# Kernel tuning notes

Hardware: AMD Instinct MI355X
Metric: run time of the kernel (lower is better)

## Reference

```python
import jax, jax.numpy as jnp
import numpy as np

N = 50000        # nodes
E = 1_600_000    # edges (avg degree 32)
H = 4            # attention heads
DPH = 32         # dims per head
D = H * DPH      # hidden/output dim = 128
IN_DIM = 5
NEG_SLOPE = 0.2
LN_EPS = 1e-5


def _glorot(key, shape):
    fan_in = shape[0] if len(shape) > 1 else shape[-1]
    return jax.random.normal(key, shape, jnp.float32) / jnp.sqrt(jnp.float32(fan_in))


def setup_inputs() -> dict:
    key = jax.random.key(0)
    ks = jax.random.split(key, 24)
    inp = {
        'x': jax.random.normal(ks[0], (N, IN_DIM), jnp.float32),
        'w_in': _glorot(ks[1], (IN_DIM, D)),
        'b_in': jnp.zeros((D,), jnp.float32),
    }
    for i in range(3):
        k = 2 + 6 * i
        inp[f'w{i}'] = _glorot(ks[k], (D, D))            # GAT linear
        inp[f'asrc{i}'] = _glorot(ks[k + 1], (H, DPH))   # att_src
        inp[f'adst{i}'] = _glorot(ks[k + 2], (H, DPH))   # att_dst
        inp[f'cb{i}'] = jnp.zeros((D,), jnp.float32)     # conv bias
        inp[f'g{i}'] = jnp.ones((D,), jnp.float32)       # LN gamma
        inp[f'lb{i}'] = jnp.zeros((D,), jnp.float32)     # LN beta
    inp['edge_index'] = jax.random.randint(ks[23], (2, E), 0, N, dtype=jnp.int32)
    return inp


def _gat_layer(h, src, dst, W, a_src, a_dst, bias):
    # h: [N, D]; src/dst: [E+N] (self loops included)
    xh = (h @ W).reshape(N, H, DPH)                      # [N, H, DPH]
    al_s = jnp.einsum('nhd,hd->nh', xh, a_src)           # [N, H]
    al_d = jnp.einsum('nhd,hd->nh', xh, a_dst)
    e = jax.nn.leaky_relu(al_s[src] + al_d[dst], NEG_SLOPE)   # [E', H]
    m = jax.ops.segment_max(e, dst, num_segments=N)      # segment softmax over incoming edges
    ex = jnp.exp(e - m[dst])
    denom = jax.ops.segment_sum(ex, dst, num_segments=N)
    alpha = ex / (denom[dst] + 1e-16)                    # [E', H]
    out = jax.ops.segment_sum(xh[src] * alpha[..., None], dst, num_segments=N)
    return out.reshape(N, D) + bias


def _layer_norm(x, g, b):
    mu = jnp.mean(x, axis=-1, keepdims=True)
    var = jnp.mean((x - mu) ** 2, axis=-1, keepdims=True)
    return (x - mu) * jax.lax.rsqrt(var + LN_EPS) * g + b


def reference(x, w_in, b_in,
              w0, asrc0, adst0, cb0, g0, lb0,
              w1, asrc1, adst1, cb1, g1, lb1,
              w2, asrc2, adst2, cb2, g2, lb2,
              edge_index):
    loops = jnp.arange(N, dtype=edge_index.dtype)
    src = jnp.concatenate([edge_index[0], loops])        # PyG GATConv add_self_loops=True
    dst = jnp.concatenate([edge_index[1], loops])
    h = x @ w_in + b_in                                  # [N, D]
    layers = [(w0, asrc0, adst0, cb0, g0, lb0),
              (w1, asrc1, adst1, cb1, g1, lb1),
              (w2, asrc2, adst2, cb2, g2, lb2)]
    for i, (W, a_s, a_d, cb, g, lb) in enumerate(layers):
        h_new = _gat_layer(h, src, dst, W, a_s, a_d, cb)
        h_new = _layer_norm(h_new, g, lb)
        if i < 2:
            h_new = jax.nn.relu(h_new)                   # dropout = identity in eval
        h = h + h_new                                    # dims always match (128)
    return h
```

## Files before the change

kernel.cpp:

```cpp
#include <hip/hip_runtime.h>

#define NN 50000
#define NE 1600000
#define EP (NE + NN)
#define D 128
#define H 4
#define NEG 0.2f
#define LN_EPS 1e-5f
#define NBUCK 49
#define BCAP 40960
#define CHUNK 4096

typedef _Float16 f16;
typedef _Float16 half8 __attribute__((ext_vector_type(8)));
typedef _Float16 half2v __attribute__((ext_vector_type(2)));
typedef float f32x4v __attribute__((ext_vector_type(4)));
typedef unsigned short u16;
typedef unsigned int u32;

static __device__ __forceinline__ float leakyf(float v) { return fmaxf(v, NEG * v); }

static __device__ __forceinline__ int fkey(float v) {
    int b = __float_as_int(v);
    return b >= 0 ? b : (b ^ 0x7fffffff);
}
static __device__ __forceinline__ float fdec(int k) {
    return __int_as_float(k >= 0 ? k : (k ^ 0x7fffffff));
}
#define NEG_INF_KEY 0x807fffff

__global__ void k_init(int* __restrict__ deg, int* __restrict__ gmaxk,
                       int* __restrict__ gcur,
                       const float* __restrict__ w0, const float* __restrict__ w1,
                       const float* __restrict__ w2, f16* __restrict__ wt,
                       const float* __restrict__ as0, const float* __restrict__ ad0,
                       const float* __restrict__ as1, const float* __restrict__ ad1,
                       const float* __restrict__ as2, const float* __restrict__ ad2,
                       f16* __restrict__ ws16) {
    int t = blockIdx.x * blockDim.x + threadIdx.x;
    if (t < NN) deg[t] = 0;
    if (t < 12) gmaxk[t] = NEG_INF_KEY;
    if (t < NBUCK) gcur[t] = 0;
    int u = t - 50176;
    if (u >= 0 && u < 3 * D * D) {
        int l = u / (D * D), rem = u % (D * D);
        int k = rem >> 7, c = rem & 127;
        const float* w = (l == 0) ? w0 : (l == 1) ? w1 : w2;
        wt[l * D * D + c * D + k] = (f16)w[rem];
    }
    int v = t - 99328;
    if (v >= 0 && v < 3 * 16 * D) {
        int l = v / (16 * D), rem = v % (16 * D);
        int c = rem >> 7, k = rem & 127;
        f16 out = (f16)0.f;
        if (c < 8) {
            int head = c >> 1;
            const float* w = (l == 0) ? w0 : (l == 1) ? w1 : w2;
            const float* av = (c & 1) ? ((l == 0) ? ad0 : (l == 1) ? ad1 : ad2)
                                      : ((l == 0) ? as0 : (l == 1) ? as1 : as2);
            float s = 0.f;
#pragma unroll
            for (int j = 0; j < 32; j++)
                s = fmaf(w[k * D + head * 32 + j], av[head * 32 + j], s);
            out = (f16)s;
        }
        ws16[l * 16 * D + c * D + k] = out;
    }
}

__global__ __launch_bounds__(256) void k_bin(const int* __restrict__ ei,
                                             int* __restrict__ gcur,
                                             u32* __restrict__ binned) {
    __shared__ u32 pk[CHUNK];
    __shared__ int hist[NBUCK], base[NBUCK], lcur[NBUCK];
    int tid = threadIdx.x;
    int cbase = blockIdx.x * CHUNK;
    if (tid < NBUCK) hist[tid] = 0;
    __syncthreads();
#pragma unroll
    for (int j = 0; j < CHUNK / 256; j++) {
        int k = cbase + j * 256 + tid;
        u32 v = 0xFFFFFFFFu;
        if (k < EP) {
            int src, dst;
            if (k < NE) { src = ei[k]; dst = ei[NE + k]; }
            else        { src = k - NE; dst = src; }
            v = ((u32)dst << 16) | (u32)src;
            atomicAdd(&hist[dst >> 10], 1);
        }
        pk[j * 256 + tid] = v;
    }
    __syncthreads();
    if (tid < NBUCK) {
        base[tid] = atomicAdd(&gcur[tid], hist[tid]);
        lcur[tid] = 0;
    }
    __syncthreads();
#pragma unroll
    for (int j = 0; j < CHUNK / 256; j++) {
        u32 v = pk[j * 256 + tid];
        if (v != 0xFFFFFFFFu) {
            int b = v >> 26;
            int pos = base[b] + atomicAdd(&lcur[b], 1);
            binned[(size_t)b * BCAP + pos] = v;
        }
    }
}

__global__ __launch_bounds__(1024) void k_cnt2(const int* __restrict__ gcur,
                                               const u32* __restrict__ binned,
                                               int* __restrict__ deg) {
    __shared__ int hist[1024];
    int b = blockIdx.x >> 2, sub = blockIdx.x & 3;
    hist[threadIdx.x] = 0;
    __syncthreads();
    int cnt = gcur[b];
    const u32* bb = binned + (size_t)b * BCAP;
    for (int i = sub * 1024 + threadIdx.x; i < cnt; i += 4096)
        atomicAdd(&hist[(bb[i] >> 16) & 1023], 1);
    __syncthreads();
    int n = (b << 10) + threadIdx.x;
    if (n < NN && hist[threadIdx.x]) atomicAdd(&deg[n], hist[threadIdx.x]);
}

#define SCAN_B 512
__global__ void k_scan1(const int* __restrict__ deg, int* __restrict__ stmp, int* __restrict__ bsum) {
    __shared__ int sm[SCAN_B];
    int i = blockIdx.x * SCAN_B + threadIdx.x;
    sm[threadIdx.x] = (i < NN) ? ((deg[i] + 7) & ~7) : 0;
    __syncthreads();
    for (int off = 1; off < SCAN_B; off <<= 1) {
        int t = (threadIdx.x >= off) ? sm[threadIdx.x - off] : 0;
        __syncthreads();
        sm[threadIdx.x] += t;
        __syncthreads();
    }
    if (i < NN) stmp[i] = sm[threadIdx.x];
    if (threadIdx.x == SCAN_B - 1) bsum[blockIdx.x] = sm[SCAN_B - 1];
}

__global__ void k_scan2(int* __restrict__ bsum, int nb) {
    __shared__ int sm[256];
    int v = (threadIdx.x < nb) ? bsum[threadIdx.x] : 0;
    sm[threadIdx.x] = v;
    __syncthreads();
    for (int off = 1; off < 256; off <<= 1) {
        int t = (threadIdx.x >= off) ? sm[threadIdx.x - off] : 0;
        __syncthreads();
        sm[threadIdx.x] += t;
        __syncthreads();
    }
    if (threadIdx.x < nb) bsum[threadIdx.x] = sm[threadIdx.x];
}

__global__ void k_scan3(const int* __restrict__ stmp, const int* __restrict__ bsum,
                        const int* __restrict__ deg, int* __restrict__ rowptr,
                        int* __restrict__ cur, u16* __restrict__ csr) {
    int i = blockIdx.x * SCAN_B + threadIdx.x;
    if (i >= NN) return;
    int add = (blockIdx.x > 0) ? bsum[blockIdx.x - 1] : 0;
    int end = stmp[i] + add;
    rowptr[i + 1] = end;
    if (i == 0) rowptr[0] = 0;
    int d = deg[i];
    int start = end - ((d + 7) & ~7);
    cur[i] = start;
    for (int j = start + d; j < end; ++j) csr[j] = 0xFFFFu;
}

__global__ __launch_bounds__(1024) void k_scatter(const int* __restrict__ gcur,
                                                  int* __restrict__ cur,
                                                  const u32* __restrict__ binned,
                                                  u16* __restrict__ csr) {
    int b = blockIdx.x >> 2, sub = blockIdx.x & 3;
    int cnt = gcur[b];
    const u32* bb = binned + (size_t)b * BCAP;
    for (int i = sub * 1024 + threadIdx.x; i < cnt; i += 4096) {
        u32 v = bb[i];
        int dst = v >> 16;
        int pos = atomicAdd(&cur[dst], 1);
        csr[pos] = (u16)(v & 0xFFFFu);
    }
}

__global__ void k_in(const float* __restrict__ x, const float* __restrict__ w,
                     const float* __restrict__ b, f16* __restrict__ h16) {
    int t = blockIdx.x * blockDim.x + threadIdx.x;
    if (t >= NN * D) return;
    int n = t >> 7, d = t & 127;
    const float* xr = x + n * 5;
    float acc = b[d];
#pragma unroll
    for (int k = 0; k < 5; k++) acc = fmaf(xr[k], w[k * D + d], acc);
    h16[t] = (f16)acc;
}

__global__ __launch_bounds__(256) void k_gemm(const f16* __restrict__ h16,
                                              const f16* __restrict__ wt,
                                              const f16* __restrict__ ws16,
                                              f16* __restrict__ xh,
                                              float* __restrict__ als,
                                              float* __restrict__ ald,
                                              int* __restrict__ gmaxk) {
    __shared__ int sgk[4];
    if (threadIdx.x < 4) sgk[threadIdx.x] = NEG_INF_KEY;
    int wid = threadIdx.x >> 6;
    int lane = threadIdx.x & 63;
    int wbase = blockIdx.x * 128 + wid * 32;
    int r = lane & 15;
    int g = lane >> 4;

    int arow0 = wbase + r;      if (arow0 >= NN) arow0 = NN - 1;
    int arow1 = wbase + 16 + r; if (arow1 >= NN) arow1 = NN - 1;
    const f16* a0p = h16 + (size_t)arow0 * D + g * 8;
    const f16* a1p = h16 + (size_t)arow1 * D + g * 8;

    f32x4v acc0[8], acc1[8], al0, al1;
#pragma unroll
    for (int nt = 0; nt < 8; nt++) {
        acc0[nt] = (f32x4v){0.f, 0.f, 0.f, 0.f};
        acc1[nt] = (f32x4v){0.f, 0.f, 0.f, 0.f};
    }
    al0 = (f32x4v){0.f, 0.f, 0.f, 0.f};
    al1 = (f32x4v){0.f, 0.f, 0.f, 0.f};

#pragma unroll
    for (int ks = 0; ks < 4; ks++) {
        half8 a0 = *(const half8*)(a0p + ks * 32);
        half8 a1 = *(const half8*)(a1p + ks * 32);
        half8 bal = *(const half8*)(ws16 + (size_t)r * D + ks * 32 + g * 8);
        al0 = __builtin_amdgcn_mfma_f32_16x16x32_f16(a0, bal, al0, 0, 0, 0);
        al1 = __builtin_amdgcn_mfma_f32_16x16x32_f16(a1, bal, al1, 0, 0, 0);
#pragma unroll
        for (int nt = 0; nt < 8; nt++) {
            half8 b = *(const half8*)(wt + (size_t)(nt * 16 + r) * D + ks * 32 + g * 8);
            acc0[nt] = __builtin_amdgcn_mfma_f32_16x16x32_f16(a0, b, acc0[nt], 0, 0, 0);
            acc1[nt] = __builtin_amdgcn_mfma_f32_16x16x32_f16(a1, b, acc1[nt], 0, 0, 0);
        }
    }

#pragma unroll
    for (int rg = 0; rg < 4; rg++) {
        int n0 = wbase + g * 4 + rg;
        if (n0 < NN) {
#pragma unroll
            for (int nt = 0; nt < 8; nt++)
                xh[(size_t)n0 * D + nt * 16 + r] = (f16)acc0[nt][rg];
        }
        int n1 = wbase + 16 + g * 4 + rg;
        if (n1 < NN) {
#pragma unroll
            for (int nt = 0; nt < 8; nt++)
                xh[(size_t)n1 * D + nt * 16 + r] = (f16)acc1[nt][rg];
        }
    }

    float m = -1e30f;
#pragma unroll
    for (int rg = 0; rg < 4; rg++) {
        int n0 = wbase + g * 4 + rg;
        int n1 = wbase + 16 + g * 4 + rg;
        float v0 = al0[rg], v1 = al1[rg];
        if (r < 8) {
            int hh = r >> 1;
            if (r & 1) {
                if (n0 < NN) ald[n0 * H + hh] = v0;
                if (n1 < NN) ald[n1 * H + hh] = v1;
            } else {
                if (n0 < NN) als[n0 * H + hh] = v0;
                if (n1 < NN) als[n1 * H + hh] = v1;
                m = fmaxf(m, fmaxf(v0, v1));
            }
        }
    }
    m = fmaxf(m, __shfl_xor(m, 16));
    m = fmaxf(m, __shfl_xor(m, 32));
    __syncthreads();
    if (lane < 8 && !(r & 1)) atomicMax(&sgk[r >> 1], fkey(m));
    __syncthreads();
    if (threadIdx.x < 4) atomicMax(&gmaxk[threadIdx.x], sgk[threadIdx.x]);
}

__global__ __launch_bounds__(256) void k_agg(const f16* __restrict__ xh,
                                             const float* __restrict__ als,
                                             const float* __restrict__ ald,
                                             const int* __restrict__ gmaxk,
                                             const int* __restrict__ rp,
                                             const u16* __restrict__ csr,
                                             const float* __restrict__ cb,
                                             const float* __restrict__ gamma,
                                             const float* __restrict__ beta,
                                             f16* __restrict__ h16,
                                             float* __restrict__ hout, int do_relu) {
    int node = blockIdx.x * 4 + (threadIdx.x >> 6);
    if (node >= NN) return;
    int lane = threadIdx.x & 63;
    int slot = lane >> 4;
    int q = lane & 15;
    int head = q >> 2;
    unsigned qo = q * 8;

    int start = rp[node], end = rp[node + 1];

    float adH = ald[node * H + head];
    float mH = leakyf(fdec(gmaxk[head]) + adH);

    float acc[8];
#pragma unroll
    for (int j = 0; j < 8; j++) acc[j] = 0.f;
    float den = 0.f;

    int sh = (slot & 1) << 4;
    bool hiw = (slot & 2) != 0;

    for (int e = start; e < end; e += 8) {
        uint4 cw = *(const uint4*)(csr + e);
        unsigned dw0 = hiw ? cw.y : cw.x;
        unsigned dw1 = hiw ? cw.w : cw.z;
        unsigned s0 = (dw0 >> sh) & 0xffffu;
        unsigned s1 = (dw1 >> sh) & 0xffffu;
        bool v0 = s0 != 0xffffu;
        bool v1 = s1 != 0xffffu;
        unsigned sc0 = v0 ? s0 : 0u;
        unsigned sc1 = v1 ? s1 : 0u;
        float al0 = als[sc0 * 4u + (unsigned)head];
        float al1 = als[sc1 * 4u + (unsigned)head];
        float ev0 = v0 ? __expf(leakyf(al0 + adH) - mH) : 0.f;
        float ev1 = v1 ? __expf(leakyf(al1 + adH) - mH) : 0.f;
        den += ev0 + ev1;
        half8 p0 = *(const half8*)(xh + sc0 * 128u + qo);
        half8 p1 = *(const half8*)(xh + sc1 * 128u + qo);
#pragma unroll
        for (int j = 0; j < 8; j++)
            acc[j] = fmaf(ev0, (float)p0[j], fmaf(ev1, (float)p1[j], acc[j]));
    }

    den += __shfl_xor(den, 16);
    den += __shfl_xor(den, 32);
#pragma unroll
    for (int j = 0; j < 8; j++) {
        acc[j] += __shfl_xor(acc[j], 16);
        acc[j] += __shfl_xor(acc[j], 32);
    }

    float inv_den = 1.f / (den + 1e-16f);
    float o[8];
    const float4* cb4 = (const float4*)(cb + q * 8);
    float4 cba = cb4[0], cbb = cb4[1];
    o[0] = fmaf(acc[0], inv_den, cba.x);
    o[1] = fmaf(acc[1], inv_den, cba.y);
    o[2] = fmaf(acc[2], inv_den, cba.z);
    o[3] = fmaf(acc[3], inv_den, cba.w);
    o[4] = fmaf(acc[4], inv_den, cbb.x);
    o[5] = fmaf(acc[5], inv_den, cbb.y);
    o[6] = fmaf(acc[6], inv_den, cbb.z);
    o[7] = fmaf(acc[7], inv_den, cbb.w);

    float s = 0.f;
#pragma unroll
    for (int j = 0; j < 8; j++) s += o[j];
#pragma unroll
    for (int off = 1; off < 16; off <<= 1) s += __shfl_xor(s, off);
    float mean = s * (1.f / 128.f);
    float v = 0.f;
    float c[8];
#pragma unroll
    for (int j = 0; j < 8; j++) { c[j] = o[j] - mean; v = fmaf(c[j], c[j], v); }
#pragma unroll
    for (int off = 1; off < 16; off <<= 1) v += __shfl_xor(v, off);
    float inv = rsqrtf(v * (1.f / 128.f) + LN_EPS);

    int dim = q * 8 + slot * 2;
    float2 g2 = *(const float2*)(gamma + dim);
    float2 b2 = *(const float2*)(beta + dim);
    float r0 = c[slot * 2] * inv * g2.x + b2.x;
    float r1 = c[slot * 2 + 1] * inv * g2.y + b2.y;
    if (do_relu) { r0 = fmaxf(r0, 0.f); r1 = fmaxf(r1, 0.f); }
    half2v hv16 = *(const half2v*)&h16[(size_t)node * D + dim];
    float n0 = (float)hv16[0] + r0;
    float n1 = (float)hv16[1] + r1;
    if (do_relu) {
        half2v h2; h2[0] = (f16)n0; h2[1] = (f16)n1;
        *(half2v*)&h16[(size_t)node * D + dim] = h2;
    } else {
        *(float2*)&hout[(size_t)node * D + dim] = (float2){n0, n1};
    }
}

extern "C" void kernel_launch(void* const* d_in, const int* in_sizes, int n_in,
                              void* d_out, int out_size, void* d_ws, size_t ws_size,
                              hipStream_t stream) {
    const float* x    = (const float*)d_in[0];
    const float* w_in = (const float*)d_in[1];
    const float* b_in = (const float*)d_in[2];
    const int*   ei   = (const int*)d_in[21];
    float* hout = (float*)d_out;

    char* w = (char*)d_ws;
    int* deg    = (int*)w;  w += (size_t)NN * 4;
    int* cur    = (int*)w;  w += (size_t)NN * 4;
    int* stmp   = (int*)w;  w += (size_t)NN * 4;
    int* bsum   = (int*)w;  w += 1024;
    int* rowptr = (int*)w;  w += (size_t)(NN + 8) * 4;
    int* gmaxk  = (int*)w;  w += 64;
    int* gcur   = (int*)w;  w += 256;
    u16* csr    = (u16*)w;  w += (size_t)(EP + 7 * NN + 64) * 2;
    f16* h16    = (f16*)w;  w += (size_t)NN * D * 2;
    f16* xh     = (f16*)w;  w += (size_t)NN * D * 2;
    f16* wt     = (f16*)w;  w += (size_t)3 * D * D * 2;
    f16* ws16   = (f16*)w;  w += (size_t)3 * 16 * D * 2;
    float* als  = (float*)w; w += (size_t)NN * H * 4;
    float* ald  = (float*)w; w += (size_t)NN * H * 4;
    u32* binned = (u32*)h16;

    k_init<<<412, 256, 0, stream>>>(deg, gmaxk, gcur,
                                    (const float*)d_in[3], (const float*)d_in[9],
                                    (const float*)d_in[15], wt,
                                    (const float*)d_in[4], (const float*)d_in[5],
                                    (const float*)d_in[10], (const float*)d_in[11],
                                    (const float*)d_in[16], (const float*)d_in[17],
                                    ws16);
    k_bin<<<(EP + CHUNK - 1) / CHUNK, 256, 0, stream>>>(ei, gcur, binned);
    k_cnt2<<<NBUCK * 4, 1024, 0, stream>>>(gcur, binned, deg);
    int nbScan = (NN + SCAN_B - 1) / SCAN_B;
    k_scan1<<<nbScan, SCAN_B, 0, stream>>>(deg, stmp, bsum);
    k_scan2<<<1, 256, 0, stream>>>(bsum, nbScan);
    k_scan3<<<nbScan, SCAN_B, 0, stream>>>(stmp, bsum, deg, rowptr, cur, csr);
    k_scatter<<<NBUCK * 4, 1024, 0, stream>>>(gcur, cur, binned, csr);

    k_in<<<(NN * D) / 256, 256, 0, stream>>>(x, w_in, b_in, h16);

    for (int L = 0; L < 3; ++L) {
        const float* cb   = (const float*)d_in[6 + 6 * L];
        const float* g    = (const float*)d_in[7 + 6 * L];
        const float* lb   = (const float*)d_in[8 + 6 * L];
        k_gemm<<<(NN + 127) / 128, 256, 0, stream>>>(h16, wt + (size_t)L * D * D,
                                                     ws16 + (size_t)L * 16 * D,
                                                     xh, als, ald, gmaxk + 4 * L);
        k_agg<<<(NN + 3) / 4, 256, 0, stream>>>(xh, als, ald, gmaxk + 4 * L, rowptr, csr,
                                                cb, g, lb, h16, hout, L < 2 ? 1 : 0);
    }
}
```

Baseline: 399.4 us.

## Collapse CSR build into one per-bucket kernel and fuse prep kernels

Merges edge binning, weight transposition, attention-weight folding and the input projection into one multi-role launch. It replaces the separate count, three-pass scan and scatter kernels with a single per-bucket kernel that does a local histogram, an in-block scan and a shared-memory-atomic scatter into fixed-capacity bucket regions. Row pointers become int2 start/end pairs. The aim is fewer launches and no global degree atomics or global scan, at the cost of padded per-bucket CSR storage and only 49 blocks in the build step.

```diff
diff --git a/kernel.cpp b/kernel.cpp
--- a/kernel.cpp
+++ b/kernel.cpp
@@ -9,6 +9,7 @@
 #define LN_EPS 1e-5f
 #define NBUCK 49
 #define BCAP 40960
+#define BCAPC 49152
 #define CHUNK 4096
 
 typedef _Float16 f16;
@@ -29,27 +30,75 @@
 }
 #define NEG_INF_KEY 0x807fffff
 
-__global__ void k_init(int* __restrict__ deg, int* __restrict__ gmaxk,
-                       int* __restrict__ gcur,
-                       const float* __restrict__ w0, const float* __restrict__ w1,
-                       const float* __restrict__ w2, f16* __restrict__ wt,
-                       const float* __restrict__ as0, const float* __restrict__ ad0,
-                       const float* __restrict__ as1, const float* __restrict__ ad1,
-                       const float* __restrict__ as2, const float* __restrict__ ad2,
-                       f16* __restrict__ ws16) {
-    int t = blockIdx.x * blockDim.x + threadIdx.x;
-    if (t < NN) deg[t] = 0;
+__global__ void k_init(int* __restrict__ gcur, int* __restrict__ gmaxk) {
+    int t = threadIdx.x;
+    if (t < NBUCK) gcur[t] = 0;
     if (t < 12) gmaxk[t] = NEG_INF_KEY;
-    if (t < NBUCK) gcur[t] = 0;
-    int u = t - 50176;
-    if (u >= 0 && u < 3 * D * D) {
+}
+
+#define BIN_BLKS 403
+#define WT_BLKS 192
+#define WS_BLKS 24
+#define KIN_BLKS 3125
+__global__ __launch_bounds__(256) void k_binfat(
+        const int* __restrict__ ei, int* __restrict__ gcur, u32* __restrict__ binned,
+        const float* __restrict__ w0, const float* __restrict__ w1,
+        const float* __restrict__ w2, f16* __restrict__ wt,
+        const float* __restrict__ as0, const float* __restrict__ ad0,
+        const float* __restrict__ as1, const float* __restrict__ ad1,
+        const float* __restrict__ as2, const float* __restrict__ ad2,
+        f16* __restrict__ ws16,
+        const float* __restrict__ x, const float* __restrict__ w_in,
+        const float* __restrict__ b_in, f16* __restrict__ h16) {
+    __shared__ u32 pk[CHUNK];
+    __shared__ int hist[NBUCK], base[NBUCK], lcur[NBUCK];
+    int tid = threadIdx.x;
+    int bid = blockIdx.x;
+
+    if (bid < BIN_BLKS) {
+        int cbase = bid * CHUNK;
+        if (tid < NBUCK) hist[tid] = 0;
+        __syncthreads();
+#pragma unroll
+        for (int j = 0; j < CHUNK / 256; j++) {
+            int k = cbase + j * 256 + tid;
+            u32 v = 0xFFFFFFFFu;
+            if (k < EP) {
+                int src, dst;
+                if (k < NE) { src = ei[k]; dst = ei[NE + k]; }
+                else        { src = k - NE; dst = src; }
+                v = ((u32)dst << 16) | (u32)src;
+                atomicAdd(&hist[dst >> 10], 1);
+            }
+            pk[j * 256 + tid] = v;
+        }
+        __syncthreads();
+        if (tid < NBUCK) {
+            base[tid] = atomicAdd(&gcur[tid], hist[tid]);
+            lcur[tid] = 0;
+        }
+        __syncthreads();
+#pragma unroll
+        for (int j = 0; j < CHUNK / 256; j++) {
+            u32 v = pk[j * 256 + tid];
+            if (v != 0xFFFFFFFFu) {
+                int b = v >> 26;
+                int pos = base[b] + atomicAdd(&lcur[b], 1);
+                binned[(size_t)b * BCAP + pos] = v;
+            }
+        }
+        return;
+    }
+    if (bid < BIN_BLKS + WT_BLKS) {
+        int u = (bid - BIN_BLKS) * 256 + tid;
         int l = u / (D * D), rem = u % (D * D);
         int k = rem >> 7, c = rem & 127;
         const float* w = (l == 0) ? w0 : (l == 1) ? w1 : w2;
         wt[l * D * D + c * D + k] = (f16)w[rem];
-    }
-    int v = t - 99328;
-    if (v >= 0 && v < 3 * 16 * D) {
+        return;
+    }
+    if (bid < BIN_BLKS + WT_BLKS + WS_BLKS) {
+        int v = (bid - BIN_BLKS - WT_BLKS) * 256 + tid;
         int l = v / (16 * D), rem = v % (16 * D);
         int c = rem >> 7, k = rem & 127;
         f16 out = (f16)0.f;
@@ -65,134 +114,65 @@
             out = (f16)s;
         }
         ws16[l * 16 * D + c * D + k] = out;
-    }
-}
-
-__global__ __launch_bounds__(256) void k_bin(const int* __restrict__ ei,
-                                             int* __restrict__ gcur,
-                                             u32* __restrict__ binned) {
-    __shared__ u32 pk[CHUNK];
-    __shared__ int hist[NBUCK], base[NBUCK], lcur[NBUCK];
+        return;
+    }
+    int gid = (bid - BIN_BLKS - WT_BLKS - WS_BLKS) * 256 + tid;
+    int n = gid >> 4;
+    int d0 = (gid & 15) << 3;
+    const float* xr = x + n * 5;
+    float x0 = xr[0], x1 = xr[1], x2 = xr[2], x3 = xr[3], x4 = xr[4];
+    half8 hv;
+#pragma unroll
+    for (int j = 0; j < 8; j++) {
+        int d = d0 + j;
+        float acc = b_in[d];
+        acc = fmaf(x0, w_in[0 * D + d], acc);
+        acc = fmaf(x1, w_in[1 * D + d], acc);
+        acc = fmaf(x2, w_in[2 * D + d], acc);
+        acc = fmaf(x3, w_in[3 * D + d], acc);
+        acc = fmaf(x4, w_in[4 * D + d], acc);
+        hv[j] = (f16)acc;
+    }
+    *(half8*)&h16[(size_t)n * D + d0] = hv;
+}
+
+__global__ __launch_bounds__(1024) void k_build(const int* __restrict__ gcur,
+                                                const u32* __restrict__ binned,
+                                                int2* __restrict__ rps,
+                                                u16* __restrict__ csr) {
+    __shared__ int hist[1024];
+    __shared__ int sm[1024];
     int tid = threadIdx.x;
-    int cbase = blockIdx.x * CHUNK;
-    if (tid < NBUCK) hist[tid] = 0;
-    __syncthreads();
-#pragma unroll
-    for (int j = 0; j < CHUNK / 256; j++) {
-        int k = cbase + j * 256 + tid;
-        u32 v = 0xFFFFFFFFu;
-        if (k < EP) {
-            int src, dst;
-            if (k < NE) { src = ei[k]; dst = ei[NE + k]; }
-            else        { src = k - NE; dst = src; }
-            v = ((u32)dst << 16) | (u32)src;
-            atomicAdd(&hist[dst >> 10], 1);
-        }
-        pk[j * 256 + tid] = v;
-    }
-    __syncthreads();
-    if (tid < NBUCK) {
-        base[tid] = atomicAdd(&gcur[tid], hist[tid]);
-        lcur[tid] = 0;
-    }
-    __syncthreads();
-#pragma unroll
-    for (int j = 0; j < CHUNK / 256; j++) {
-        u32 v = pk[j * 256 + tid];
-        if (v != 0xFFFFFFFFu) {
-            int b = v >> 26;
-            int pos = base[b] + atomicAdd(&lcur[b], 1);
-            binned[(size_t)b * BCAP + pos] = v;
-        }
-    }
-}
-
-__global__ __launch_bounds__(1024) void k_cnt2(const int* __restrict__ gcur,
-                                               const u32* __restrict__ binned,
-                                               int* __restrict__ deg) {
-    __shared__ int hist[1024];
-    int b = blockIdx.x >> 2, sub = blockIdx.x & 3;
-    hist[threadIdx.x] = 0;
+    int b = blockIdx.x;
+    hist[tid] = 0;
     __syncthreads();
     int cnt = gcur[b];
     const u32* bb = binned + (size_t)b * BCAP;
-    for (int i = sub * 1024 + threadIdx.x; i < cnt; i += 4096)
+    for (int i = tid; i < cnt; i += 1024)
         atomicAdd(&hist[(bb[i] >> 16) & 1023], 1);
     __syncthreads();
-    int n = (b << 10) + threadIdx.x;
-    if (n < NN && hist[threadIdx.x]) atomicAdd(&deg[n], hist[threadIdx.x]);
-}
-
-#define SCAN_B 512
-__global__ void k_scan1(const int* __restrict__ deg, int* __restrict__ stmp, int* __restrict__ bsum) {
-    __shared__ int sm[SCAN_B];
-    int i = blockIdx.x * SCAN_B + threadIdx.x;
-    sm[threadIdx.x] = (i < NN) ? ((deg[i] + 7) & ~7) : 0;
-    __syncthreads();
-    for (int off = 1; off < SCAN_B; off <<= 1) {
-        int t = (threadIdx.x >= off) ? sm[threadIdx.x - off] : 0;
+    int d = hist[tid];
+    int pd = (d + 7) & ~7;
+    sm[tid] = pd;
+    __syncthreads();
+    for (int off = 1; off < 1024; off <<= 1) {
+        int t = (tid >= off) ? sm[tid - off] : 0;
         __syncthreads();
-        sm[threadIdx.x] += t;
+        sm[tid] += t;
         __syncthreads();
     }
-    if (i < NN) stmp[i] = sm[threadIdx.x];
-    if (threadIdx.x == SCAN_B - 1) bsum[blockIdx.x] = sm[SCAN_B - 1];
-}
-
-__global__ void k_scan2(int* __restrict__ bsum, int nb) {
-    __shared__ int sm[256];
-    int v = (threadIdx.x < nb) ? bsum[threadIdx.x] : 0;
-    sm[threadIdx.x] = v;
-    __syncthreads();
-    for (int off = 1; off < 256; off <<= 1) {
-        int t = (threadIdx.x >= off) ? sm[threadIdx.x - off] : 0;
-        __syncthreads();
-        sm[threadIdx.x] += t;
-        __syncthreads();
-    }
-    if (threadIdx.x < nb) bsum[threadIdx.x] = sm[threadIdx.x];
-}
-
-__global__ void k_scan3(const int* __restrict__ stmp, const int* __restrict__ bsum,
-                        const int* __restrict__ deg, int* __restrict__ rowptr,
-                        int* __restrict__ cur, u16* __restrict__ csr) {
-    int i = blockIdx.x * SCAN_B + threadIdx.x;
-    if (i >= NN) return;
-    int add = (blockIdx.x > 0) ? bsum[blockIdx.x - 1] : 0;
-    int end = stmp[i] + add;
-    rowptr[i + 1] = end;
-    if (i == 0) rowptr[0] = 0;
-    int d = deg[i];
-    int start = end - ((d + 7) & ~7);
-    cur[i] = start;
-    for (int j = start + d; j < end; ++j) csr[j] = 0xFFFFu;
-}
-
-__global__ __launch_bounds__(1024) void k_scatter(const int* __restrict__ gcur,
-                                                  int* __restrict__ cur,
-                                                  const u32* __restrict__ binned,
-                                                  u16* __restrict__ csr) {
-    int b = blockIdx.x >> 2, sub = blockIdx.x & 3;
-    int cnt = gcur[b];
-    const u32* bb = binned + (size_t)b * BCAP;
-    for (int i = sub * 1024 + threadIdx.x; i < cnt; i += 4096) {
+    int basep = b * BCAPC + sm[tid] - pd;
+    int node = (b << 10) + tid;
+    if (node < NN) rps[node] = make_int2(basep, basep + pd);
+    for (int j = d; j < pd; ++j) csr[basep + j] = 0xFFFFu;
+    __syncthreads();
+    hist[tid] = basep;
+    __syncthreads();
+    for (int i = tid; i < cnt; i += 1024) {
         u32 v = bb[i];
-        int dst = v >> 16;
-        int pos = atomicAdd(&cur[dst], 1);
+        int pos = atomicAdd(&hist[(v >> 16) & 1023], 1);
         csr[pos] = (u16)(v & 0xFFFFu);
     }
-}
-
-__global__ void k_in(const float* __restrict__ x, const float* __restrict__ w,
-                     const float* __restrict__ b, f16* __restrict__ h16) {
-    int t = blockIdx.x * blockDim.x + threadIdx.x;
-    if (t >= NN * D) return;
-    int n = t >> 7, d = t & 127;
-    const float* xr = x + n * 5;
-    float acc = b[d];
-#pragma unroll
-    for (int k = 0; k < 5; k++) acc = fmaf(xr[k], w[k * D + d], acc);
-    h16[t] = (f16)acc;
 }
 
 __global__ __launch_bounds__(256) void k_gemm(const f16* __restrict__ h16,
@@ -285,7 +265,7 @@
                                              const float* __restrict__ als,
                                              const float* __restrict__ ald,
                                              const int* __restrict__ gmaxk,
-                                             const int* __restrict__ rp,
+                                             const int2* __restrict__ rps,
                                              const u16* __restrict__ csr,
                                              const float* __restrict__ cb,
                                              const float* __restrict__ gamma,
@@ -300,7 +280,8 @@
     int head = q >> 2;
     unsigned qo = q * 8;
 
-    int start = rp[node], end = rp[node + 1];
+    int2 se = rps[node];
+    int start = se.x, end = se.y;
 
     float adH = ald[node * H + head];
     float mH = leakyf(fdec(gmaxk[head]) + adH);
@@ -397,38 +378,27 @@
     float* hout = (float*)d_out;
 
     char* w = (char*)d_ws;
-    int* deg    = (int*)w;  w += (size_t)NN * 4;
-    int* cur    = (int*)w;  w += (size_t)NN * 4;
-    int* stmp   = (int*)w;  w += (size_t)NN * 4;
-    int* bsum   = (int*)w;  w += 1024;
-    int* rowptr = (int*)w;  w += (size_t)(NN + 8) * 4;
-    int* gmaxk  = (int*)w;  w += 64;
-    int* gcur   = (int*)w;  w += 256;
-    u16* csr    = (u16*)w;  w += (size_t)(EP + 7 * NN + 64) * 2;
-    f16* h16    = (f16*)w;  w += (size_t)NN * D * 2;
-    f16* xh     = (f16*)w;  w += (size_t)NN * D * 2;
-    f16* wt     = (f16*)w;  w += (size_t)3 * D * D * 2;
-    f16* ws16   = (f16*)w;  w += (size_t)3 * 16 * D * 2;
+    int* gmaxk  = (int*)w;   w += 64;
+    int* gcur   = (int*)w;   w += 256;
+    int2* rps   = (int2*)w;  w += (size_t)NN * 8;
+    u16* csr    = (u16*)w;   w += (size_t)NBUCK * BCAPC * 2;
+    f16* h16    = (f16*)w;   w += (size_t)NN * D * 2;
+    f16* xh     = (f16*)w;   w += (size_t)NN * D * 2;
+    f16* wt     = (f16*)w;   w += (size_t)3 * D * D * 2;
+    f16* ws16   = (f16*)w;   w += (size_t)3 * 16 * D * 2;
     float* als  = (float*)w; w += (size_t)NN * H * 4;
     float* ald  = (float*)w; w += (size_t)NN * H * 4;
-    u32* binned = (u32*)h16;
-
-    k_init<<<412, 256, 0, stream>>>(deg, gmaxk, gcur,
-                                    (const float*)d_in[3], (const float*)d_in[9],
-                                    (const float*)d_in[15], wt,
-                                    (const float*)d_in[4], (const float*)d_in[5],
-                                    (const float*)d_in[10], (const float*)d_in[11],
-                                    (const float*)d_in[16], (const float*)d_in[17],
-                                    ws16);
-    k_bin<<<(EP + CHUNK - 1) / CHUNK, 256, 0, stream>>>(ei, gcur, binned);
-    k_cnt2<<<NBUCK * 4, 1024, 0, stream>>>(gcur, binned, deg);
-    int nbScan = (NN + SCAN_B - 1) / SCAN_B;
-    k_scan1<<<nbScan, SCAN_B, 0, stream>>>(deg, stmp, bsum);
-    k_scan2<<<1, 256, 0, stream>>>(bsum, nbScan);
-    k_scan3<<<nbScan, SCAN_B, 0, stream>>>(stmp, bsum, deg, rowptr, cur, csr);
-    k_scatter<<<NBUCK * 4, 1024, 0, stream>>>(gcur, cur, binned, csr);
-
-    k_in<<<(NN * D) / 256, 256, 0, stream>>>(x, w_in, b_in, h16);
+    u32* binned = (u32*)xh;
+
+    k_init<<<1, 64, 0, stream>>>(gcur, gmaxk);
+    k_binfat<<<BIN_BLKS + WT_BLKS + WS_BLKS + KIN_BLKS, 256, 0, stream>>>(
+        ei, gcur, binned,
+        (const float*)d_in[3], (const float*)d_in[9], (const float*)d_in[15], wt,
+        (const float*)d_in[4], (const float*)d_in[5],
+        (const float*)d_in[10], (const float*)d_in[11],
+        (const float*)d_in[16], (const float*)d_in[17], ws16,
+        x, w_in, b_in, h16);
+    k_build<<<NBUCK, 1024, 0, stream>>>(gcur, binned, rps, csr);
 
     for (int L = 0; L < 3; ++L) {
         const float* cb   = (const float*)d_in[6 + 6 * L];
@@ -437,7 +407,7 @@
         k_gemm<<<(NN + 127) / 128, 256, 0, stream>>>(h16, wt + (size_t)L * D * D,
                                                      ws16 + (size_t)L * 16 * D,
                                                      xh, als, ald, gmaxk + 4 * L);
-        k_agg<<<(NN + 3) / 4, 256, 0, stream>>>(xh, als, ald, gmaxk + 4 * L, rowptr, csr,
+        k_agg<<<(NN + 3) / 4, 256, 0, stream>>>(xh, als, ald, gmaxk + 4 * L, rps, csr,
                                                 cb, g, lb, h16, hout, L < 2 ? 1 : 0);
     }
 }
```

Measured after the change: 359.4 us. 10.0% less time.
